# Kernel optimization log

Measured on AMD Instinct MI355X. Metric: run time of the kernel, lower is better.

The kernel has to match this reference:

```python
import jax, jax.numpy as jnp
import numpy as np

BN_EPS = 1e-5
LN_EPS = 1e-5

N_NODES = 50000
N_EDGES = 800000
D_IN = 128
D_HID = 512


def _batchnorm(h, gamma, beta):
    # training-mode BatchNorm1d: biased variance over the node/batch dim
    m = jnp.mean(h, axis=0)
    v = jnp.mean(jnp.square(h - m), axis=0)
    return (h - m) * jax.lax.rsqrt(v + BN_EPS) * gamma + beta


def setup_inputs() -> dict:
    key = jax.random.key(0)
    ks = jax.random.split(key, 8)
    x = jax.random.normal(ks[0], (N_NODES, D_IN), dtype=jnp.float32)
    edge_index = jax.random.randint(ks[1], (2, N_EDGES), 0, N_NODES, dtype=jnp.int64)
    s1 = 1.0 / np.sqrt(D_IN)
    s2 = 1.0 / np.sqrt(D_HID)
    W1 = jax.random.uniform(ks[2], (D_IN, D_HID), jnp.float32, -s1, s1)
    b1 = jax.random.uniform(ks[3], (D_HID,), jnp.float32, -s1, s1)
    W2 = jax.random.uniform(ks[4], (D_HID, D_IN), jnp.float32, -s2, s2)
    b2 = jax.random.uniform(ks[5], (D_IN,), jnp.float32, -s2, s2)
    return {
        "x": x,
        "edge_index": edge_index,
        "W1": W1, "b1": b1,
        "bn1_g": jnp.ones((D_HID,), jnp.float32), "bn1_b": jnp.zeros((D_HID,), jnp.float32),
        "W2": W2, "b2": b2,
        "bn2_g": jnp.ones((D_IN,), jnp.float32), "bn2_b": jnp.zeros((D_IN,), jnp.float32),
        "ln_g": jnp.ones((D_IN,), jnp.float32), "ln_b": jnp.zeros((D_IN,), jnp.float32),
    }


def reference(x, edge_index, W1, b1, bn1_g, bn1_b, W2, b2, bn2_g, bn2_b, ln_g, ln_b):
    n = x.shape[0]
    src = edge_index[0]
    dst = edge_index[1]
    # GIN aggregation: sum of neighbor (source) features at each destination node
    agg = jax.ops.segment_sum(x[src], dst, num_segments=n)  # [N, D_IN]
    h = x + agg  # (1 + eps) * x + agg, eps = 0
    # MLP: Linear -> BN -> ReLU -> Linear -> BN -> ReLU (final activation)
    h = jax.nn.relu(_batchnorm(h @ W1 + b1, bn1_g, bn1_b))  # [N, D_HID]
    h = jax.nn.relu(_batchnorm(h @ W2 + b2, bn2_g, bn2_b))  # [N, D_IN]
    # residual + LayerNorm (dropout p=0 -> identity)
    out = h + x
    m = jnp.mean(out, axis=-1, keepdims=True)
    v = jnp.mean(jnp.square(out - m), axis=-1, keepdims=True)
    out = (out - m) * jax.lax.rsqrt(v + LN_EPS) * ln_g + ln_b
    return out
```

## Files before the change

kernel.cpp:

```cpp
#include <hip/hip_runtime.h>
#include <stdint.h>

#define N_NODES 50000
#define N_EDGES 800000
#define D_IN    128
#define D_HID   512
#define NPAD    50048
#define SCAN_NB 196

typedef __attribute__((ext_vector_type(8))) short short8;
typedef __attribute__((ext_vector_type(4))) float f32x4;

union Pack8 { unsigned short us[8]; uint4 v; };

__device__ __forceinline__ float bf2f(unsigned short u) {
    union { unsigned int i; float f; } v; v.i = ((unsigned int)u) << 16; return v.f;
}
__device__ __forceinline__ unsigned short f2bf(float f) {
    union { float f; unsigned int i; } v; v.f = f;
    unsigned int r = v.i + 0x7fffu + ((v.i >> 16) & 1u);
    return (unsigned short)(r >> 16);
}
__device__ __forceinline__ float loadP(const void* p, long i, int isf) {
    return isf ? ((const float*)p)[i] : bf2f(((const unsigned short*)p)[i]);
}
__device__ __forceinline__ uint4 pack8(float4 f0, float4 f1) {
    Pack8 p;
    p.us[0] = f2bf(f0.x); p.us[1] = f2bf(f0.y); p.us[2] = f2bf(f0.z); p.us[3] = f2bf(f0.w);
    p.us[4] = f2bf(f1.x); p.us[5] = f2bf(f1.y); p.us[6] = f2bf(f1.z); p.us[7] = f2bf(f1.w);
    return p.v;
}

__global__ void k_init(const void* __restrict__ x, const int* __restrict__ ei,
                       float* __restrict__ stats, int* __restrict__ counts,
                       int* __restrict__ flags) {
    int t = threadIdx.x;
    if (blockIdx.x < 201) {
        int i = blockIdx.x * 256 + t;
        if (i < 1280) stats[i] = 0.f;
        else if (i < 1280 + N_NODES) counts[i - 1280] = 0;
    } else {
        __shared__ int sh[2];
        if (t == 0) { sh[0] = 0; sh[1] = 1; }
        __syncthreads();
        const unsigned short* xu = (const unsigned short*)x;
        for (int i = t; i < 8192; i += 256)
            if (((xu[i] >> 7) & 0xFF) == 0xFF) sh[0] = 1;
        for (int k = t; k < 64; k += 256)
            if (ei[2 * k + 1] != 0) sh[1] = 0;
        __syncthreads();
        if (t == 0) { flags[0] = sh[0]; flags[1] = sh[1]; }
    }
}

__global__ void k_transpose2(const void* __restrict__ W1, const void* __restrict__ W2,
                             unsigned short* __restrict__ w1t, unsigned short* __restrict__ w2t,
                             const int* __restrict__ flags) {
    int isf = flags[0];
    int idx = blockIdx.x * 256 + threadIdx.x;
    if (idx < D_IN * D_HID) {
        int k = idx / D_HID, n = idx % D_HID;
        w1t[n * D_IN + k] = isf ? f2bf(((const float*)W1)[idx])
                                : ((const unsigned short*)W1)[idx];
    } else {
        int j = idx - D_IN * D_HID;
        int k = j / D_IN, n = j % D_IN;
        w2t[n * D_HID + k] = isf ? f2bf(((const float*)W2)[j])
                                 : ((const unsigned short*)W2)[j];
    }
}

__global__ void k_count(const int* __restrict__ ei, int* __restrict__ counts,
                        const int* __restrict__ flags) {
    int i64 = flags[1];
    int e = blockIdx.x * 256 + threadIdx.x;
    int d = i64 ? ei[2 * N_EDGES + 2 * e] : ei[N_EDGES + e];
    d = min(max(d, 0), N_NODES - 1);
    atomicAdd(&counts[d], 1);
}

__global__ __launch_bounds__(256) void k_scan_block(const int* __restrict__ counts,
                                                    int* __restrict__ rowptr,
                                                    int* __restrict__ partials) {
    __shared__ int a[256], b[256];
    int t = threadIdx.x;
    int idx = blockIdx.x * 256 + t;
    int c = (idx < N_NODES) ? counts[idx] : 0;
    a[t] = c;
    __syncthreads();
    int* src = a; int* dst = b;
    for (int off = 1; off < 256; off <<= 1) {
        dst[t] = src[t] + ((t >= off) ? src[t - off] : 0);
        __syncthreads();
        int* tmp = src; src = dst; dst = tmp;
    }
    if (idx < N_NODES) rowptr[idx] = src[t] - c;
    if (t == 255) partials[blockIdx.x] = src[255];
}

__global__ __launch_bounds__(256) void k_scan_part(int* __restrict__ partials) {
    __shared__ int a[256], b[256];
    int t = threadIdx.x;
    int c = (t < SCAN_NB) ? partials[t] : 0;
    a[t] = c;
    __syncthreads();
    int* src = a; int* dst = b;
    for (int off = 1; off < 256; off <<= 1) {
        dst[t] = src[t] + ((t >= off) ? src[t - off] : 0);
        __syncthreads();
        int* tmp = src; src = dst; dst = tmp;
    }
    if (t < SCAN_NB) partials[t] = src[t] - c;
}

__global__ void k_scan_add(int* __restrict__ rowptr, int* __restrict__ cursor,
                           const int* __restrict__ partials) {
    int idx = blockIdx.x * 256 + threadIdx.x;
    if (idx < N_NODES) {
        int v = rowptr[idx] + partials[blockIdx.x];
        rowptr[idx] = v;
        cursor[idx] = v;
    } else if (idx == N_NODES) {
        rowptr[N_NODES] = N_EDGES;
    }
}

__global__ void k_fill(const int* __restrict__ ei, int* __restrict__ cursor,
                       int* __restrict__ bucket, const int* __restrict__ flags) {
    int i64 = flags[1];
    int e = blockIdx.x * 256 + threadIdx.x;
    int s, d;
    if (i64) { s = ei[2 * e]; d = ei[2 * N_EDGES + 2 * e]; }
    else     { s = ei[e];     d = ei[N_EDGES + e]; }
    s = min(max(s, 0), N_NODES - 1);
    d = min(max(d, 0), N_NODES - 1);
    int pos = atomicAdd(&cursor[d], 1);
    bucket[pos] = s;
}

__global__ __launch_bounds__(256) void k_gather(const int* __restrict__ rowptr,
                                                const int* __restrict__ bucket,
                                                const void* __restrict__ x,
                                                float* __restrict__ agg,
                                                const int* __restrict__ flags) {
    int isf = flags[0];
    int w = threadIdx.x >> 6, lane = threadIdx.x & 63;
    int row = blockIdx.x * 4 + w;
    float a0 = 0.f, a1 = 0.f;
    if (row < N_NODES) {
        int beg = rowptr[row], end = rowptr[row + 1];
        if (isf) {
            const float* xf = (const float*)x;
            float2 v = *(const float2*)(xf + (size_t)row * D_IN + lane * 2);
            a0 = v.x; a1 = v.y;
            int j = beg;
            for (; j + 4 <= end; j += 4) {
                int s0 = bucket[j], s1 = bucket[j + 1], s2 = bucket[j + 2], s3 = bucket[j + 3];
                float2 n0 = *(const float2*)(xf + (size_t)s0 * D_IN + lane * 2);
                float2 n1 = *(const float2*)(xf + (size_t)s1 * D_IN + lane * 2);
                float2 n2 = *(const float2*)(xf + (size_t)s2 * D_IN + lane * 2);
                float2 n3 = *(const float2*)(xf + (size_t)s3 * D_IN + lane * 2);
                a0 += (n0.x + n1.x) + (n2.x + n3.x);
                a1 += (n0.y + n1.y) + (n2.y + n3.y);
            }
            for (; j < end; j++) {
                float2 n = *(const float2*)(xf + (size_t)bucket[j] * D_IN + lane * 2);
                a0 += n.x; a1 += n.y;
            }
        } else {
            const unsigned int* xu = (const unsigned int*)x;
            unsigned int u = xu[(size_t)row * 64 + lane];
            a0 = bf2f(u & 0xffff); a1 = bf2f(u >> 16);
            int j = beg;
            for (; j + 4 <= end; j += 4) {
                int s0 = bucket[j], s1 = bucket[j + 1], s2 = bucket[j + 2], s3 = bucket[j + 3];
                unsigned int u0 = xu[(size_t)s0 * 64 + lane];
                unsigned int u1 = xu[(size_t)s1 * 64 + lane];
                unsigned int u2 = xu[(size_t)s2 * 64 + lane];
                unsigned int u3 = xu[(size_t)s3 * 64 + lane];
                a0 += (bf2f(u0 & 0xffff) + bf2f(u1 & 0xffff)) + (bf2f(u2 & 0xffff) + bf2f(u3 & 0xffff));
                a1 += (bf2f(u0 >> 16) + bf2f(u1 >> 16)) + (bf2f(u2 >> 16) + bf2f(u3 >> 16));
            }
            for (; j < end; j++) {
                unsigned int n = xu[(size_t)bucket[j] * 64 + lane];
                a0 += bf2f(n & 0xffff); a1 += bf2f(n >> 16);
            }
        }
    }
    *(float2*)(agg + (size_t)row * D_IN + lane * 2) = make_float2(a0, a1);
}

__global__ __launch_bounds__(256) void k_g1stats(const float* __restrict__ agg,
                                                 const unsigned short* __restrict__ w1t,
                                                 const void* __restrict__ b1,
                                                 float* __restrict__ sum1,
                                                 float* __restrict__ sumsq1,
                                                 const int* __restrict__ flags) {
    __shared__ unsigned short ldsX[128 * 128];
    __shared__ unsigned short ldsW[128 * 128];
    int isf = flags[0];
    int t = threadIdx.x;
    int m0 = blockIdx.x * 128;
    int r = t >> 1, half = t & 1;
#pragma unroll
    for (int i = 0; i < 8; i++) {
        int chunk = half * 8 + i;
        int sw = ((chunk ^ (r & 15)) * 8);
        const float* g = agg + (size_t)(m0 + r) * D_IN + chunk * 8;
        *(uint4*)(ldsX + r * 128 + sw) = pack8(*(const float4*)g, *(const float4*)(g + 4));
    }
    int wid = t >> 6, lane = t & 63;
    int wm = wid & 1, wn = wid >> 1;
    int quad = lane >> 4, l16 = lane & 15;
    for (int nb = 0; nb < 4; nb++) {
        __syncthreads();
#pragma unroll
        for (int i = 0; i < 8; i++) {
            int chunk = half * 8 + i;
            *(uint4*)(ldsW + r * 128 + ((chunk ^ (r & 15)) * 8)) =
                *(const uint4*)(w1t + (size_t)(nb * 128 + r) * D_IN + chunk * 8);
        }
        __syncthreads();
        f32x4 acc[4][4] = {};
#pragma unroll
        for (int ks = 0; ks < 4; ks++) {
            short8 af[4], bfr[4];
#pragma unroll
            for (int mt = 0; mt < 4; mt++)
                af[mt] = *(const short8*)(ldsX + (wm * 64 + mt * 16 + l16) * 128 + (((ks * 4 + quad) ^ l16) * 8));
#pragma unroll
            for (int nt = 0; nt < 4; nt++)
                bfr[nt] = *(const short8*)(ldsW + (wn * 64 + nt * 16 + l16) * 128 + (((ks * 4 + quad) ^ l16) * 8));
#pragma unroll
            for (int mt = 0; mt < 4; mt++)
#pragma unroll
                for (int nt = 0; nt < 4; nt++)
                    acc[mt][nt] = __builtin_amdgcn_mfma_f32_16x16x32_bf16(af[mt], bfr[nt], acc[mt][nt], 0, 0, 0);
        }
#pragma unroll
        for (int nt = 0; nt < 4; nt++) {
            int n = nb * 128 + wn * 64 + nt * 16 + l16;
            float bias = loadP(b1, n, isf);
            float s = 0.f, ss = 0.f;
#pragma unroll
            for (int mt = 0; mt < 4; mt++) {
                int Rb = m0 + wm * 64 + mt * 16 + quad * 4;
#pragma unroll
                for (int rg = 0; rg < 4; rg++) {
                    if (Rb + rg < N_NODES) {
                        float z = acc[mt][nt][rg] + bias;
                        s += z; ss += z * z;
                    }
                }
            }
            s += __shfl_xor(s, 16, 64); ss += __shfl_xor(ss, 16, 64);
            s += __shfl_xor(s, 32, 64); ss += __shfl_xor(ss, 32, 64);
            if (quad == 0) { atomicAdd(&sum1[n], s); atomicAdd(&sumsq1[n], ss); }
        }
    }
}

__global__ __launch_bounds__(256) void k_fused(const float* __restrict__ agg,
                                               const unsigned short* __restrict__ w1t,
                                               const unsigned short* __restrict__ w2t,
                                               const void* __restrict__ b1,
                                               const void* __restrict__ b2,
                                               const void* __restrict__ g1,
                                               const void* __restrict__ bb1,
                                               const float* __restrict__ sum1,
                                               const float* __restrict__ sumsq1,
                                               float* __restrict__ h2,
                                               float* __restrict__ sum2,
                                               float* __restrict__ sumsq2,
                                               const int* __restrict__ flags) {
    __shared__ unsigned short bufXP[128 * 128];
    __shared__ unsigned short bufW[128 * 128];
    int isf = flags[0];
    int t = threadIdx.x;
    int m0 = blockIdx.x * 128;
    int r = t >> 1, half = t & 1;
    int wid = t >> 6, lane = t & 63;
    int wm = wid & 1, wn = wid >> 1;
    int quad = lane >> 4, l16 = lane & 15;
    f32x4 acc2[4][4] = {};
    for (int nb = 0; nb < 4; nb++) {
        __syncthreads();
#pragma unroll
        for (int i = 0; i < 8; i++) {
            int chunk = half * 8 + i;
            int sw = ((chunk ^ (r & 15)) * 8);
            const float* g = agg + (size_t)(m0 + r) * D_IN + chunk * 8;
            *(uint4*)(bufXP + r * 128 + sw) = pack8(*(const float4*)g, *(const float4*)(g + 4));
            *(uint4*)(bufW + r * 128 + sw) = *(const uint4*)(w1t + (size_t)(nb * 128 + r) * D_IN + chunk * 8);
        }
        __syncthreads();
        f32x4 acc1[4][4] = {};
#pragma unroll
        for (int ks = 0; ks < 4; ks++) {
            short8 af[4], bfr[4];
#pragma unroll
            for (int mt = 0; mt < 4; mt++)
                af[mt] = *(const short8*)(bufXP + (wm * 64 + mt * 16 + l16) * 128 + (((ks * 4 + quad) ^ l16) * 8));
#pragma unroll
            for (int nt = 0; nt < 4; nt++)
                bfr[nt] = *(const short8*)(bufW + (wn * 64 + nt * 16 + l16) * 128 + (((ks * 4 + quad) ^ l16) * 8));
#pragma unroll
            for (int mt = 0; mt < 4; mt++)
#pragma unroll
                for (int nt = 0; nt < 4; nt++)
                    acc1[mt][nt] = __builtin_amdgcn_mfma_f32_16x16x32_bf16(af[mt], bfr[nt], acc1[mt][nt], 0, 0, 0);
        }
        __syncthreads();
#pragma unroll
        for (int nt = 0; nt < 4; nt++) {
            int nl = wn * 64 + nt * 16 + l16;
            int n1 = nb * 128 + nl;
            float mz = sum1[n1] * (1.f / N_NODES);
            float vz = sumsq1[n1] * (1.f / N_NODES) - mz * mz;
            float inv = rsqrtf(fmaxf(vz, 0.f) + 1e-5f);
            float A = loadP(g1, n1, isf) * inv;
            float C = loadP(bb1, n1, isf) - mz * A + loadP(b1, n1, isf) * A;
            int ccw = nl >> 3, cl = nl & 7;
#pragma unroll
            for (int mt = 0; mt < 4; mt++)
#pragma unroll
                for (int rg = 0; rg < 4; rg++) {
                    int R = wm * 64 + mt * 16 + quad * 4 + rg;
                    float z = fmaxf(acc1[mt][nt][rg] * A + C, 0.f);
                    bufXP[R * 128 + ((ccw ^ (R & 15)) * 8) + cl] = f2bf(z);
                }
        }
#pragma unroll
        for (int i = 0; i < 8; i++) {
            int chunk = half * 8 + i;
            *(uint4*)(bufW + r * 128 + ((chunk ^ (r & 15)) * 8)) =
                *(const uint4*)(w2t + (size_t)r * D_HID + nb * 128 + chunk * 8);
        }
        __syncthreads();
#pragma unroll
        for (int ks = 0; ks < 4; ks++) {
            short8 af[4], bfr[4];
#pragma unroll
            for (int mt = 0; mt < 4; mt++)
                af[mt] = *(const short8*)(bufXP + (wm * 64 + mt * 16 + l16) * 128 + (((ks * 4 + quad) ^ l16) * 8));
#pragma unroll
            for (int nt = 0; nt < 4; nt++)
                bfr[nt] = *(const short8*)(bufW + (wn * 64 + nt * 16 + l16) * 128 + (((ks * 4 + quad) ^ l16) * 8));
#pragma unroll
            for (int mt = 0; mt < 4; mt++)
#pragma unroll
                for (int nt = 0; nt < 4; nt++)
                    acc2[mt][nt] = __builtin_amdgcn_mfma_f32_16x16x32_bf16(af[mt], bfr[nt], acc2[mt][nt], 0, 0, 0);
        }
    }
#pragma unroll
    for (int nt = 0; nt < 4; nt++) {
        int n = wn * 64 + nt * 16 + l16;
        float bias = loadP(b2, n, isf);
        float s = 0.f, ss = 0.f;
#pragma unroll
        for (int mt = 0; mt < 4; mt++) {
            int Rb = m0 + wm * 64 + mt * 16 + quad * 4;
#pragma unroll
            for (int rg = 0; rg < 4; rg++) {
                float z = acc2[mt][nt][rg] + bias;
                h2[(size_t)(Rb + rg) * D_IN + n] = z;
                if (Rb + rg < N_NODES) { s += z; ss += z * z; }
            }
        }
        s += __shfl_xor(s, 16, 64); ss += __shfl_xor(ss, 16, 64);
        s += __shfl_xor(s, 32, 64); ss += __shfl_xor(ss, 32, 64);
        if (quad == 0) { atomicAdd(&sum2[n], s); atomicAdd(&sumsq2[n], ss); }
    }
}

__global__ __launch_bounds__(256) void k_final(const float* __restrict__ h2,
                                               const void* __restrict__ x,
                                               const float* __restrict__ sum2,
                                               const float* __restrict__ sumsq2,
                                               const void* __restrict__ g2,
                                               const void* __restrict__ bb2,
                                               const void* __restrict__ lng,
                                               const void* __restrict__ lnb,
                                               void* __restrict__ out,
                                               const int* __restrict__ flags) {
    int isf = flags[0];
    __shared__ float a2s[D_IN], c2s[D_IN];
    int t = threadIdx.x;
    if (t < D_IN) {
        float m = sum2[t] * (1.f / N_NODES);
        float v = sumsq2[t] * (1.f / N_NODES) - m * m;
        float inv = rsqrtf(fmaxf(v, 0.f) + 1e-5f);
        float a = loadP(g2, t, isf) * inv;
        a2s[t] = a;
        c2s[t] = loadP(bb2, t, isf) - m * a;
    }
    __syncthreads();
    int w = t >> 6, lane = t & 63;
    int row = blockIdx.x * 4 + w;
    if (row >= N_NODES) return;
    size_t base = (size_t)row * D_IN;
    float o0 = fmaxf(a2s[lane] * h2[base + lane] + c2s[lane], 0.f) + loadP(x, base + lane, isf);
    float o1 = fmaxf(a2s[lane + 64] * h2[base + 64 + lane] + c2s[lane + 64], 0.f) + loadP(x, base + 64 + lane, isf);
    float s = o0 + o1, ss = o0 * o0 + o1 * o1;
#pragma unroll
    for (int m = 1; m < 64; m <<= 1) {
        s += __shfl_xor(s, m, 64);
        ss += __shfl_xor(ss, m, 64);
    }
    float mean = s * (1.f / D_IN);
    float var = ss * (1.f / D_IN) - mean * mean;
    float inv = rsqrtf(fmaxf(var, 0.f) + 1e-5f);
    float r0 = (o0 - mean) * inv * loadP(lng, lane, isf) + loadP(lnb, lane, isf);
    float r1 = (o1 - mean) * inv * loadP(lng, lane + 64, isf) + loadP(lnb, lane + 64, isf);
    if (isf) {
        ((float*)out)[base + lane] = r0;
        ((float*)out)[base + 64 + lane] = r1;
    } else {
        ((unsigned short*)out)[base + lane] = f2bf(r0);
        ((unsigned short*)out)[base + 64 + lane] = f2bf(r1);
    }
}

extern "C" void kernel_launch(void* const* d_in, const int* in_sizes, int n_in,
                              void* d_out, int out_size, void* d_ws, size_t ws_size,
                              hipStream_t stream) {
    const void* x    = d_in[0];
    const int*  ei   = (const int*)d_in[1];
    const void* W1   = d_in[2];
    const void* b1   = d_in[3];
    const void* bn1g = d_in[4];
    const void* bn1b = d_in[5];
    const void* W2   = d_in[6];
    const void* b2   = d_in[7];
    const void* bn2g = d_in[8];
    const void* bn2b = d_in[9];
    const void* lng  = d_in[10];
    const void* lnb  = d_in[11];

    char* ws = (char*)d_ws;
    float* stats    = (float*)ws;
    float* sum1     = stats;
    float* sumsq1   = stats + 512;
    float* sum2     = stats + 1024;
    float* sumsq2   = stats + 1152;
    int*   flags    = (int*)(ws + 5120);
    int*   partials = (int*)(ws + 5184);
    int*   rowptr   = (int*)(ws + 8192);
    int*   cursor   = (int*)(ws + 212992);
    unsigned short* w1t = (unsigned short*)(ws + 417792);
    unsigned short* w2t = (unsigned short*)(ws + 548864);
    int*   bucket = (int*)(ws + 679936);
    float* agg    = (float*)(ws + 3879936);
    float* h2     = agg;

    k_init<<<202, 256, 0, stream>>>(x, ei, stats, cursor, flags);
    k_transpose2<<<512, 256, 0, stream>>>(W1, W2, w1t, w2t, flags);
    k_count<<<N_EDGES / 256, 256, 0, stream>>>(ei, cursor, flags);
    k_scan_block<<<SCAN_NB, 256, 0, stream>>>(cursor, rowptr, partials);
    k_scan_part<<<1, 256, 0, stream>>>(partials);
    k_scan_add<<<SCAN_NB, 256, 0, stream>>>(rowptr, cursor, partials);
    k_fill<<<N_EDGES / 256, 256, 0, stream>>>(ei, cursor, bucket, flags);
    k_gather<<<NPAD / 4, 256, 0, stream>>>(rowptr, bucket, x, agg, flags);
    k_g1stats<<<NPAD / 128, 256, 0, stream>>>(agg, w1t, b1, sum1, sumsq1, flags);
    k_fused<<<NPAD / 128, 256, 0, stream>>>(agg, w1t, w2t, b1, b2, bn1g, bn1b,
                                            sum1, sumsq1, h2, sum2, sumsq2, flags);
    k_final<<<(N_NODES + 3) / 4, 256, 0, stream>>>(h2, x, sum2, sumsq2, bn2g, bn2b, lng, lnb, d_out, flags);
}
```

Baseline: 377.6 us.

## Compute BN1 statistics via Gram matrix of aggregated features instead of full GEMM

Replaces the first-pass GEMM that computed BN1 sum and sum-of-squares with a 128x128 Gram matrix X^T X plus column sums, reduced across blocks. The per-column stats are then derived algebraically from W1. This avoids recomputing the 50000x128x512 GEMM just for statistics. The agg and h2 buffers are also stored as bf16 instead of fp32, which halves their traffic. The fused kernel keeps the A fragments in registers, and the transpose and final kernels get coalesced writes and vectorized accesses. The trade-offs are the cancellation risk of computing variance algebraically and added bf16 rounding of intermediates.

```diff
diff --git a/kernel.cpp b/kernel.cpp
--- a/kernel.cpp
+++ b/kernel.cpp
@@ -7,11 +7,11 @@
 #define D_HID   512
 #define NPAD    50048
 #define SCAN_NB 196
+#define G_TILES 782
+#define G_BLOCKS 128
 
 typedef __attribute__((ext_vector_type(8))) short short8;
 typedef __attribute__((ext_vector_type(4))) float f32x4;
-
-union Pack8 { unsigned short us[8]; uint4 v; };
 
 __device__ __forceinline__ float bf2f(unsigned short u) {
     union { unsigned int i; float f; } v; v.i = ((unsigned int)u) << 16; return v.f;
@@ -24,21 +24,15 @@
 __device__ __forceinline__ float loadP(const void* p, long i, int isf) {
     return isf ? ((const float*)p)[i] : bf2f(((const unsigned short*)p)[i]);
 }
-__device__ __forceinline__ uint4 pack8(float4 f0, float4 f1) {
-    Pack8 p;
-    p.us[0] = f2bf(f0.x); p.us[1] = f2bf(f0.y); p.us[2] = f2bf(f0.z); p.us[3] = f2bf(f0.w);
-    p.us[4] = f2bf(f1.x); p.us[5] = f2bf(f1.y); p.us[6] = f2bf(f1.z); p.us[7] = f2bf(f1.w);
-    return p.v;
-}
 
 __global__ void k_init(const void* __restrict__ x, const int* __restrict__ ei,
                        float* __restrict__ stats, int* __restrict__ counts,
                        int* __restrict__ flags) {
     int t = threadIdx.x;
-    if (blockIdx.x < 201) {
+    if (blockIdx.x < 197) {
         int i = blockIdx.x * 256 + t;
-        if (i < 1280) stats[i] = 0.f;
-        else if (i < 1280 + N_NODES) counts[i - 1280] = 0;
+        if (i < 384) stats[1024 + i] = 0.f;
+        else if (i < 384 + N_NODES) counts[i - 384] = 0;
     } else {
         __shared__ int sh[2];
         if (t == 0) { sh[0] = 0; sh[1] = 1; }
@@ -59,14 +53,16 @@
     int isf = flags[0];
     int idx = blockIdx.x * 256 + threadIdx.x;
     if (idx < D_IN * D_HID) {
-        int k = idx / D_HID, n = idx % D_HID;
-        w1t[n * D_IN + k] = isf ? f2bf(((const float*)W1)[idx])
-                                : ((const unsigned short*)W1)[idx];
+        int n = idx >> 7, k = idx & 127;
+        int src = k * D_HID + n;
+        w1t[idx] = isf ? f2bf(((const float*)W1)[src])
+                       : ((const unsigned short*)W1)[src];
     } else {
         int j = idx - D_IN * D_HID;
-        int k = j / D_IN, n = j % D_IN;
-        w2t[n * D_HID + k] = isf ? f2bf(((const float*)W2)[j])
-                                 : ((const unsigned short*)W2)[j];
+        int n = j >> 9, k = j & 511;
+        int src = k * D_IN + n;
+        w2t[j] = isf ? f2bf(((const float*)W2)[src])
+                     : ((const unsigned short*)W2)[src];
     }
 }
 
@@ -141,7 +137,7 @@
 __global__ __launch_bounds__(256) void k_gather(const int* __restrict__ rowptr,
                                                 const int* __restrict__ bucket,
                                                 const void* __restrict__ x,
-                                                float* __restrict__ agg,
+                                                unsigned short* __restrict__ agg,
                                                 const int* __restrict__ flags) {
     int isf = flags[0];
     int w = threadIdx.x >> 6, lane = threadIdx.x & 63;
@@ -187,94 +183,144 @@
             }
         }
     }
-    *(float2*)(agg + (size_t)row * D_IN + lane * 2) = make_float2(a0, a1);
-}
-
-__global__ __launch_bounds__(256) void k_g1stats(const float* __restrict__ agg,
-                                                 const unsigned short* __restrict__ w1t,
-                                                 const void* __restrict__ b1,
-                                                 float* __restrict__ sum1,
-                                                 float* __restrict__ sumsq1,
-                                                 const int* __restrict__ flags) {
-    __shared__ unsigned short ldsX[128 * 128];
-    __shared__ unsigned short ldsW[128 * 128];
-    int isf = flags[0];
+    unsigned int o = (unsigned int)f2bf(a0) | ((unsigned int)f2bf(a1) << 16);
+    ((unsigned int*)agg)[(size_t)row * 64 + lane] = o;
+}
+
+__global__ __launch_bounds__(256) void k_gram(const unsigned short* __restrict__ aggb,
+                                              float* __restrict__ Gpart,
+                                              float* __restrict__ colsum) {
+    __shared__ unsigned short ldsT[128 * 64];
     int t = threadIdx.x;
-    int m0 = blockIdx.x * 128;
-    int r = t >> 1, half = t & 1;
-#pragma unroll
-    for (int i = 0; i < 8; i++) {
-        int chunk = half * 8 + i;
-        int sw = ((chunk ^ (r & 15)) * 8);
-        const float* g = agg + (size_t)(m0 + r) * D_IN + chunk * 8;
-        *(uint4*)(ldsX + r * 128 + sw) = pack8(*(const float4*)g, *(const float4*)(g + 4));
-    }
     int wid = t >> 6, lane = t & 63;
     int wm = wid & 1, wn = wid >> 1;
     int quad = lane >> 4, l16 = lane & 15;
-    for (int nb = 0; nb < 4; nb++) {
-        __syncthreads();
-#pragma unroll
-        for (int i = 0; i < 8; i++) {
-            int chunk = half * 8 + i;
-            *(uint4*)(ldsW + r * 128 + ((chunk ^ (r & 15)) * 8)) =
-                *(const uint4*)(w1t + (size_t)(nb * 128 + r) * D_IN + chunk * 8);
-        }
-        __syncthreads();
-        f32x4 acc[4][4] = {};
-#pragma unroll
-        for (int ks = 0; ks < 4; ks++) {
-            short8 af[4], bfr[4];
+    f32x4 acc[4][4] = {};
+    float cs = 0.f;
+    int cscol = t & 127, cskh = t >> 7;
+    for (int tile = blockIdx.x; tile < G_TILES; tile += G_BLOCKS) {
+        __syncthreads();
+        size_t rowbase = (size_t)tile * 64;
+#pragma unroll
+        for (int jj = 0; jj < 2; jj++) {
+            int j = t + jj * 256;
+            int c = j >> 5, rp = j & 31;
+            uint4 v0 = *(const uint4*)(aggb + (rowbase + 2 * rp) * 128 + c * 8);
+            uint4 v1 = *(const uint4*)(aggb + (rowbase + 2 * rp + 1) * 128 + c * 8);
+            const unsigned short* p0 = (const unsigned short*)&v0;
+            const unsigned short* p1 = (const unsigned short*)&v1;
+            int k = 2 * rp, kc = k >> 3, ko = k & 7;
+#pragma unroll
+            for (int e = 0; e < 8; e++) {
+                int col = c * 8 + e;
+                *(unsigned int*)(ldsT + col * 64 + ((kc ^ (col & 7)) * 8) + ko) =
+                    (unsigned int)p0[e] | ((unsigned int)p1[e] << 16);
+            }
+        }
+        __syncthreads();
+#pragma unroll
+        for (int ksub = 0; ksub < 2; ksub++) {
+            short8 fa[4], fb[4];
+#pragma unroll
+            for (int mt = 0; mt < 4; mt++) {
+                int col = wm * 64 + mt * 16 + l16;
+                fa[mt] = *(const short8*)(ldsT + col * 64 + (((ksub * 4 + quad) ^ (col & 7)) * 8));
+            }
+#pragma unroll
+            for (int nt = 0; nt < 4; nt++) {
+                int col = wn * 64 + nt * 16 + l16;
+                fb[nt] = *(const short8*)(ldsT + col * 64 + (((ksub * 4 + quad) ^ (col & 7)) * 8));
+            }
 #pragma unroll
             for (int mt = 0; mt < 4; mt++)
-                af[mt] = *(const short8*)(ldsX + (wm * 64 + mt * 16 + l16) * 128 + (((ks * 4 + quad) ^ l16) * 8));
-#pragma unroll
-            for (int nt = 0; nt < 4; nt++)
-                bfr[nt] = *(const short8*)(ldsW + (wn * 64 + nt * 16 + l16) * 128 + (((ks * 4 + quad) ^ l16) * 8));
-#pragma unroll
-            for (int mt = 0; mt < 4; mt++)
 #pragma unroll
                 for (int nt = 0; nt < 4; nt++)
-                    acc[mt][nt] = __builtin_amdgcn_mfma_f32_16x16x32_bf16(af[mt], bfr[nt], acc[mt][nt], 0, 0, 0);
-        }
+                    acc[mt][nt] = __builtin_amdgcn_mfma_f32_16x16x32_bf16(fa[mt], fb[nt], acc[mt][nt], 0, 0, 0);
+        }
+#pragma unroll
+        for (int kc = 0; kc < 4; kc++) {
+            short8 v = *(const short8*)(ldsT + cscol * 64 + (((cskh * 4 + kc) ^ (cscol & 7)) * 8));
+#pragma unroll
+            for (int e = 0; e < 8; e++) cs += bf2f((unsigned short)v[e]);
+        }
+    }
+    float* gp = Gpart + (size_t)blockIdx.x * 16384;
+#pragma unroll
+    for (int mt = 0; mt < 4; mt++)
 #pragma unroll
         for (int nt = 0; nt < 4; nt++) {
-            int n = nb * 128 + wn * 64 + nt * 16 + l16;
-            float bias = loadP(b1, n, isf);
-            float s = 0.f, ss = 0.f;
-#pragma unroll
-            for (int mt = 0; mt < 4; mt++) {
-                int Rb = m0 + wm * 64 + mt * 16 + quad * 4;
-#pragma unroll
-                for (int rg = 0; rg < 4; rg++) {
-                    if (Rb + rg < N_NODES) {
-                        float z = acc[mt][nt][rg] + bias;
-                        s += z; ss += z * z;
-                    }
-                }
-            }
-            s += __shfl_xor(s, 16, 64); ss += __shfl_xor(ss, 16, 64);
-            s += __shfl_xor(s, 32, 64); ss += __shfl_xor(ss, 32, 64);
-            if (quad == 0) { atomicAdd(&sum1[n], s); atomicAdd(&sumsq1[n], ss); }
-        }
-    }
-}
-
-__global__ __launch_bounds__(256) void k_fused(const float* __restrict__ agg,
-                                               const unsigned short* __restrict__ w1t,
-                                               const unsigned short* __restrict__ w2t,
-                                               const void* __restrict__ b1,
-                                               const void* __restrict__ b2,
-                                               const void* __restrict__ g1,
-                                               const void* __restrict__ bb1,
-                                               const float* __restrict__ sum1,
-                                               const float* __restrict__ sumsq1,
-                                               float* __restrict__ h2,
-                                               float* __restrict__ sum2,
-                                               float* __restrict__ sumsq2,
-                                               const int* __restrict__ flags) {
-    __shared__ unsigned short bufXP[128 * 128];
+            int m = wm * 64 + mt * 16 + quad * 4;
+            int n = wn * 64 + nt * 16 + l16;
+#pragma unroll
+            for (int rg = 0; rg < 4; rg++)
+                gp[(m + rg) * 128 + n] = acc[mt][nt][rg];
+        }
+    atomicAdd(&colsum[cscol], cs);
+}
+
+__global__ void k_gred(const float* __restrict__ Gpart, float* __restrict__ G) {
+    int i = blockIdx.x * 256 + threadIdx.x;
+    float s = 0.f;
+#pragma unroll 8
+    for (int b = 0; b < G_BLOCKS; b++) s += Gpart[(size_t)b * 16384 + i];
+    G[i] = s;
+}
+
+__global__ __launch_bounds__(256) void k_bn1(const float* __restrict__ G,
+                                             const float* __restrict__ colsum,
+                                             const unsigned short* __restrict__ w1t,
+                                             const void* __restrict__ b1,
+                                             float* __restrict__ sum1,
+                                             float* __restrict__ sumsq1,
+                                             const int* __restrict__ flags) {
+    int isf = flags[0];
+    __shared__ float wsh[4][128];
+    int t = threadIdx.x, wid = t >> 6, lane = t & 63;
+    int n = blockIdx.x * 4 + wid;
+    unsigned int u = *(const unsigned int*)(w1t + (size_t)n * 128 + lane * 2);
+    wsh[wid][lane * 2] = bf2f(u & 0xffff);
+    wsh[wid][lane * 2 + 1] = bf2f(u >> 16);
+    __syncthreads();
+    const float* w = wsh[wid];
+    const f32x4* g0 = (const f32x4*)(G + (size_t)lane * 128);
+    const f32x4* g1 = (const f32x4*)(G + (size_t)(lane + 64) * 128);
+    float t0 = 0.f, t1 = 0.f;
+#pragma unroll 4
+    for (int q4 = 0; q4 < 32; q4++) {
+        f32x4 a = g0[q4], b = g1[q4];
+        float w0 = w[q4 * 4], w1 = w[q4 * 4 + 1], w2 = w[q4 * 4 + 2], w3 = w[q4 * 4 + 3];
+        t0 += a[0] * w0 + a[1] * w1 + a[2] * w2 + a[3] * w3;
+        t1 += b[0] * w0 + b[1] * w1 + b[2] * w2 + b[3] * w3;
+    }
+    float sq = w[lane] * t0 + w[lane + 64] * t1;
+    float s  = w[lane] * colsum[lane] + w[lane + 64] * colsum[lane + 64];
+#pragma unroll
+    for (int m = 1; m < 64; m <<= 1) {
+        sq += __shfl_xor(sq, m, 64);
+        s  += __shfl_xor(s, m, 64);
+    }
+    if (lane == 0) {
+        float b = loadP(b1, n, isf);
+        sum1[n]   = s + (float)N_NODES * b;
+        sumsq1[n] = sq + 2.f * b * s + (float)N_NODES * b * b;
+    }
+}
+
+__global__ __launch_bounds__(256, 2) void k_fused(const unsigned short* aggb,
+                                                  const unsigned short* __restrict__ w1t,
+                                                  const unsigned short* __restrict__ w2t,
+                                                  const void* __restrict__ b1,
+                                                  const void* __restrict__ b2,
+                                                  const void* __restrict__ g1,
+                                                  const void* __restrict__ bb1,
+                                                  const float* __restrict__ sum1,
+                                                  const float* __restrict__ sumsq1,
+                                                  unsigned short* h2,
+                                                  float* __restrict__ sum2,
+                                                  float* __restrict__ sumsq2,
+                                                  const int* __restrict__ flags) {
     __shared__ unsigned short bufW[128 * 128];
+    __shared__ unsigned short bufA[128 * 128];
     int isf = flags[0];
     int t = threadIdx.x;
     int m0 = blockIdx.x * 128;
@@ -282,35 +328,42 @@
     int wid = t >> 6, lane = t & 63;
     int wm = wid & 1, wn = wid >> 1;
     int quad = lane >> 4, l16 = lane & 15;
+#pragma unroll
+    for (int i = 0; i < 8; i++) {
+        int chunk = half * 8 + i;
+        *(uint4*)(bufA + r * 128 + ((chunk ^ (r & 15)) * 8)) =
+            *(const uint4*)(aggb + (size_t)(m0 + r) * 128 + chunk * 8);
+    }
+    __syncthreads();
+    short8 ax[4][4];
+#pragma unroll
+    for (int ks = 0; ks < 4; ks++)
+#pragma unroll
+        for (int mt = 0; mt < 4; mt++)
+            ax[ks][mt] = *(const short8*)(bufA + (wm * 64 + mt * 16 + l16) * 128 + (((ks * 4 + quad) ^ l16) * 8));
     f32x4 acc2[4][4] = {};
     for (int nb = 0; nb < 4; nb++) {
         __syncthreads();
 #pragma unroll
         for (int i = 0; i < 8; i++) {
             int chunk = half * 8 + i;
-            int sw = ((chunk ^ (r & 15)) * 8);
-            const float* g = agg + (size_t)(m0 + r) * D_IN + chunk * 8;
-            *(uint4*)(bufXP + r * 128 + sw) = pack8(*(const float4*)g, *(const float4*)(g + 4));
-            *(uint4*)(bufW + r * 128 + sw) = *(const uint4*)(w1t + (size_t)(nb * 128 + r) * D_IN + chunk * 8);
+            *(uint4*)(bufW + r * 128 + ((chunk ^ (r & 15)) * 8)) =
+                *(const uint4*)(w1t + (size_t)(nb * 128 + r) * 128 + chunk * 8);
         }
         __syncthreads();
         f32x4 acc1[4][4] = {};
 #pragma unroll
         for (int ks = 0; ks < 4; ks++) {
-            short8 af[4], bfr[4];
+            short8 bw[4];
+#pragma unroll
+            for (int nt = 0; nt < 4; nt++)
+                bw[nt] = *(const short8*)(bufW + (wn * 64 + nt * 16 + l16) * 128 + (((ks * 4 + quad) ^ l16) * 8));
 #pragma unroll
             for (int mt = 0; mt < 4; mt++)
-                af[mt] = *(const short8*)(bufXP + (wm * 64 + mt * 16 + l16) * 128 + (((ks * 4 + quad) ^ l16) * 8));
-#pragma unroll
-            for (int nt = 0; nt < 4; nt++)
-                bfr[nt] = *(const short8*)(bufW + (wn * 64 + nt * 16 + l16) * 128 + (((ks * 4 + quad) ^ l16) * 8));
-#pragma unroll
-            for (int mt = 0; mt < 4; mt++)
 #pragma unroll
                 for (int nt = 0; nt < 4; nt++)
-                    acc1[mt][nt] = __builtin_amdgcn_mfma_f32_16x16x32_bf16(af[mt], bfr[nt], acc1[mt][nt], 0, 0, 0);
-        }
-        __syncthreads();
+                    acc1[mt][nt] = __builtin_amdgcn_mfma_f32_16x16x32_bf16(ax[ks][mt], bw[nt], acc1[mt][nt], 0, 0, 0);
+        }
 #pragma unroll
         for (int nt = 0; nt < 4; nt++) {
             int nl = wn * 64 + nt * 16 + l16;
@@ -326,10 +379,10 @@
 #pragma unroll
                 for (int rg = 0; rg < 4; rg++) {
                     int R = wm * 64 + mt * 16 + quad * 4 + rg;
-                    float z = fmaxf(acc1[mt][nt][rg] * A + C, 0.f);
-                    bufXP[R * 128 + ((ccw ^ (R & 15)) * 8) + cl] = f2bf(z);
+                    bufA[R * 128 + ((ccw ^ (R & 15)) * 8) + cl] = f2bf(fmaxf(acc1[mt][nt][rg] * A + C, 0.f));
                 }
         }
+        __syncthreads();
 #pragma unroll
         for (int i = 0; i < 8; i++) {
             int chunk = half * 8 + i;
@@ -339,18 +392,18 @@
         __syncthreads();
 #pragma unroll
         for (int ks = 0; ks < 4; ks++) {
-            short8 af[4], bfr[4];
+            short8 aa[4], bw[4];
 #pragma unroll
             for (int mt = 0; mt < 4; mt++)
-                af[mt] = *(const short8*)(bufXP + (wm * 64 + mt * 16 + l16) * 128 + (((ks * 4 + quad) ^ l16) * 8));
+                aa[mt] = *(const short8*)(bufA + (wm * 64 + mt * 16 + l16) * 128 + (((ks * 4 + quad) ^ l16) * 8));
 #pragma unroll
             for (int nt = 0; nt < 4; nt++)
-                bfr[nt] = *(const short8*)(bufW + (wn * 64 + nt * 16 + l16) * 128 + (((ks * 4 + quad) ^ l16) * 8));
+                bw[nt] = *(const short8*)(bufW + (wn * 64 + nt * 16 + l16) * 128 + (((ks * 4 + quad) ^ l16) * 8));
 #pragma unroll
             for (int mt = 0; mt < 4; mt++)
 #pragma unroll
                 for (int nt = 0; nt < 4; nt++)
-                    acc2[mt][nt] = __builtin_amdgcn_mfma_f32_16x16x32_bf16(af[mt], bfr[nt], acc2[mt][nt], 0, 0, 0);
+                    acc2[mt][nt] = __builtin_amdgcn_mfma_f32_16x16x32_bf16(aa[mt], bw[nt], acc2[mt][nt], 0, 0, 0);
         }
     }
 #pragma unroll
@@ -364,7 +417,7 @@
 #pragma unroll
             for (int rg = 0; rg < 4; rg++) {
                 float z = acc2[mt][nt][rg] + bias;
-                h2[(size_t)(Rb + rg) * D_IN + n] = z;
+                h2[(size_t)(Rb + rg) * D_IN + n] = f2bf(z);
                 if (Rb + rg < N_NODES) { s += z; ss += z * z; }
             }
         }
@@ -374,7 +427,7 @@
     }
 }
 
-__global__ __launch_bounds__(256) void k_final(const float* __restrict__ h2,
+__global__ __launch_bounds__(256) void k_final(const unsigned short* __restrict__ h2,
                                                const void* __restrict__ x,
                                                const float* __restrict__ sum2,
                                                const float* __restrict__ sumsq2,
@@ -400,8 +453,18 @@
     int row = blockIdx.x * 4 + w;
     if (row >= N_NODES) return;
     size_t base = (size_t)row * D_IN;
-    float o0 = fmaxf(a2s[lane] * h2[base + lane] + c2s[lane], 0.f) + loadP(x, base + lane, isf);
-    float o1 = fmaxf(a2s[lane + 64] * h2[base + 64 + lane] + c2s[lane + 64], 0.f) + loadP(x, base + 64 + lane, isf);
+    int c0 = lane * 2, c1 = lane * 2 + 1;
+    unsigned int hu = ((const unsigned int*)h2)[base / 2 + lane];
+    float x0, x1;
+    if (isf) {
+        float2 xv = *((const float2*)x + base / 2 + lane);
+        x0 = xv.x; x1 = xv.y;
+    } else {
+        unsigned int xu = ((const unsigned int*)x)[base / 2 + lane];
+        x0 = bf2f(xu & 0xffff); x1 = bf2f(xu >> 16);
+    }
+    float o0 = fmaxf(a2s[c0] * bf2f(hu & 0xffff) + c2s[c0], 0.f) + x0;
+    float o1 = fmaxf(a2s[c1] * bf2f(hu >> 16) + c2s[c1], 0.f) + x1;
     float s = o0 + o1, ss = o0 * o0 + o1 * o1;
 #pragma unroll
     for (int m = 1; m < 64; m <<= 1) {
@@ -411,14 +474,12 @@
     float mean = s * (1.f / D_IN);
     float var = ss * (1.f / D_IN) - mean * mean;
     float inv = rsqrtf(fmaxf(var, 0.f) + 1e-5f);
-    float r0 = (o0 - mean) * inv * loadP(lng, lane, isf) + loadP(lnb, lane, isf);
-    float r1 = (o1 - mean) * inv * loadP(lng, lane + 64, isf) + loadP(lnb, lane + 64, isf);
+    float r0 = (o0 - mean) * inv * loadP(lng, c0, isf) + loadP(lnb, c0, isf);
+    float r1 = (o1 - mean) * inv * loadP(lng, c1, isf) + loadP(lnb, c1, isf);
     if (isf) {
-        ((float*)out)[base + lane] = r0;
-        ((float*)out)[base + 64 + lane] = r1;
+        *((float2*)out + base / 2 + lane) = make_float2(r0, r1);
     } else {
-        ((unsigned short*)out)[base + lane] = f2bf(r0);
-        ((unsigned short*)out)[base + 64 + lane] = f2bf(r1);
+        ((unsigned int*)out)[base / 2 + lane] = (unsigned int)f2bf(r0) | ((unsigned int)f2bf(r1) << 16);
     }
 }
 
@@ -439,22 +500,25 @@
     const void* lnb  = d_in[11];
 
     char* ws = (char*)d_ws;
-    float* stats    = (float*)ws;
-    float* sum1     = stats;
-    float* sumsq1   = stats + 512;
-    float* sum2     = stats + 1024;
-    float* sumsq2   = stats + 1152;
-    int*   flags    = (int*)(ws + 5120);
-    int*   partials = (int*)(ws + 5184);
-    int*   rowptr   = (int*)(ws + 8192);
-    int*   cursor   = (int*)(ws + 212992);
-    unsigned short* w1t = (unsigned short*)(ws + 417792);
-    unsigned short* w2t = (unsigned short*)(ws + 548864);
-    int*   bucket = (int*)(ws + 679936);
-    float* agg    = (float*)(ws + 3879936);
-    float* h2     = agg;
-
-    k_init<<<202, 256, 0, stream>>>(x, ei, stats, cursor, flags);
+    float* stats   = (float*)ws;
+    float* sum1    = stats;
+    float* sumsq1  = stats + 512;
+    float* sum2    = stats + 1024;
+    float* sumsq2  = stats + 1152;
+    float* colsum  = stats + 1280;
+    int*   flags   = (int*)(ws + 5632);
+    int*   partials= (int*)(ws + 5696);
+    int*   rowptr  = (int*)(ws + 8192);
+    int*   cursor  = (int*)(ws + 208256);
+    unsigned short* w1t = (unsigned short*)(ws + 408320);
+    unsigned short* w2t = (unsigned short*)(ws + 539392);
+    float* G       = (float*)(ws + 670464);
+    float* Gpart   = (float*)(ws + 736000);
+    int*   bucket  = (int*)(ws + 9124608);
+    unsigned short* agg = (unsigned short*)(ws + 12324608);
+    unsigned short* h2  = agg;
+
+    k_init<<<198, 256, 0, stream>>>(x, ei, stats, cursor, flags);
     k_transpose2<<<512, 256, 0, stream>>>(W1, W2, w1t, w2t, flags);
     k_count<<<N_EDGES / 256, 256, 0, stream>>>(ei, cursor, flags);
     k_scan_block<<<SCAN_NB, 256, 0, stream>>>(cursor, rowptr, partials);
@@ -462,7 +526,9 @@
     k_scan_add<<<SCAN_NB, 256, 0, stream>>>(rowptr, cursor, partials);
     k_fill<<<N_EDGES / 256, 256, 0, stream>>>(ei, cursor, bucket, flags);
     k_gather<<<NPAD / 4, 256, 0, stream>>>(rowptr, bucket, x, agg, flags);
-    k_g1stats<<<NPAD / 128, 256, 0, stream>>>(agg, w1t, b1, sum1, sumsq1, flags);
+    k_gram<<<G_BLOCKS, 256, 0, stream>>>(agg, Gpart, colsum);
+    k_gred<<<64, 256, 0, stream>>>(Gpart, G);
+    k_bn1<<<128, 256, 0, stream>>>(G, colsum, w1t, b1, sum1, sumsq1, flags);
     k_fused<<<NPAD / 128, 256, 0, stream>>>(agg, w1t, w2t, b1, b2, bn1g, bn1b,
                                             sum1, sumsq1, h2, sum2, sumsq2, flags);
     k_final<<<(N_NODES + 3) / 4, 256, 0, stream>>>(h2, x, sum2, sumsq2, bn2g, bn2b, lng, lnb, d_out, flags);
```

New measurement: 398.8 us. 5.6% more time.
